# Optimization experiments

Measured on AMD Instinct MI355X. Metric: run time of the kernel, lower is better.

## Reference

```python
import jax, jax.numpy as jnp
import numpy as np

N, D, H = 3072, 1152, 16
HD = D // H  # 72


def setup_inputs() -> dict:
    key = jax.random.key(0)
    ks = jax.random.split(key, 12)
    w = lambda k, shp: jax.random.normal(k, shp, dtype=jnp.float32) * 0.02
    return {
        "hidden_states": jax.random.normal(ks[0], (N, D), dtype=jnp.float32),
        "rotary_pos_emb": jax.random.normal(ks[1], (N, HD // 2), dtype=jnp.float32),
        "cu_seqlens": jnp.arange(5, dtype=jnp.int32) * (N // 4),
        "wq": w(ks[2], (D, D)), "bq": jnp.zeros((D,), jnp.float32),
        "wk": w(ks[3], (D, D)), "bk": jnp.zeros((D,), jnp.float32),
        "wv": w(ks[4], (D, D)), "bv": jnp.zeros((D,), jnp.float32),
        "wo": w(ks[5], (D, D)), "bo": jnp.zeros((D,), jnp.float32),
    }


def _rotate_half(x):
    x1, x2 = jnp.split(x, 2, axis=-1)
    return jnp.concatenate((-x2, x1), axis=-1)


def _apply_rope(t, freqs):
    # t: [N, H, HD], freqs: [N, HD//2]
    cos = jnp.concatenate([jnp.cos(freqs), jnp.cos(freqs)], axis=-1)[:, None, :]  # [N,1,HD]
    sin = jnp.concatenate([jnp.sin(freqs), jnp.sin(freqs)], axis=-1)[:, None, :]
    return (t.astype(jnp.float32) * cos + _rotate_half(t.astype(jnp.float32)) * sin).astype(t.dtype)


def reference(hidden_states, rotary_pos_emb, cu_seqlens, wq, bq, wk, bk, wv, bv, wo, bo):
    n = hidden_states.shape[0]
    q = (hidden_states @ wq.T + bq).reshape(n, H, HD)
    k = (hidden_states @ wk.T + bk).reshape(n, H, HD)
    v = (hidden_states @ wv.T + bv).reshape(n, H, HD)
    q = _apply_rope(q, rotary_pos_emb)
    k = _apply_rope(k, rotary_pos_emb)
    # block-diagonal mask: same segment id (from cu_seqlens) -> attend
    seg = jnp.searchsorted(cu_seqlens, jnp.arange(n), side="right")
    same = seg[:, None] == seg[None, :]  # [N, N]
    neg = jnp.finfo(q.dtype).min
    scores = jnp.einsum("qhd,khd->hqk", q, k) / jnp.sqrt(jnp.float32(HD)).astype(q.dtype)
    scores = scores + jnp.where(same, jnp.zeros((), q.dtype), neg)[None, :, :]
    attn = jax.nn.softmax(scores.astype(jnp.float32), axis=-1).astype(q.dtype)
    out = jnp.einsum("hqk,khd->qhd", attn, v).reshape(n, D)
    return out @ wo.T + bo
```

## Files before the change

kernel.cpp:

```cpp
#include <hip/hip_runtime.h>
#include <hip/hip_bf16.h>


typedef __attribute__((ext_vector_type(8))) __bf16 bf16x8;
typedef __attribute__((ext_vector_type(4))) float f32x4;
typedef __attribute__((ext_vector_type(8))) unsigned short u16x8;
typedef __attribute__((ext_vector_type(4))) unsigned short u16x4;

#define N_TOK 3072
#define DMODEL 1152
#define NH 16
#define HDIM 72
#define SEGLEN 768

__device__ __forceinline__ unsigned short bf16rn(float f) {
  union { float f; unsigned int u; } v; v.f = f;
  return (unsigned short)((v.u + 0x7fffu + ((v.u >> 16) & 1u)) >> 16);
}
__device__ __forceinline__ float bf2f(unsigned short u) {
  union { unsigned int i; float f; } v; v.i = ((unsigned int)u) << 16;
  return v.f;
}

#define GLOAD16(gsrc, ldst)                                                  \
  __builtin_amdgcn_global_load_lds(                                         \
      (const __attribute__((address_space(1))) unsigned int*)(gsrc),        \
      (__attribute__((address_space(3))) unsigned int*)(ldst), 16, 0, 0)

__global__ __launch_bounds__(256) void prep_kernel(
    const float* __restrict__ hs,
    const float* __restrict__ wq, const float* __restrict__ wk,
    const float* __restrict__ wv, const float* __restrict__ wo,
    const float* __restrict__ bq, const float* __restrict__ bk,
    const float* __restrict__ bv,
    unsigned short* __restrict__ Xbf, unsigned short* __restrict__ Wqkv,
    unsigned short* __restrict__ Wo, float* __restrict__ biasqkv) {
  const int idx = blockIdx.x * 256 + threadIdx.x;
  const int stride = gridDim.x * 256;
  const int NX4 = (N_TOK * DMODEL) / 4;
  const int NW4 = (DMODEL * DMODEL) / 4;
  for (int i = idx; i < NX4; i += stride) {
    f32x4 v = ((const f32x4*)hs)[i];
    u16x4 o;
    for (int j = 0; j < 4; ++j) o[j] = bf16rn(v[j]);
    ((u16x4*)Xbf)[i] = o;
  }
  for (int i = idx; i < NW4; i += stride) {
    f32x4 a = ((const f32x4*)wq)[i];
    f32x4 b = ((const f32x4*)wk)[i];
    f32x4 c = ((const f32x4*)wv)[i];
    f32x4 d = ((const f32x4*)wo)[i];
    u16x4 oa, ob, oc, od;
    for (int j = 0; j < 4; ++j) {
      oa[j] = bf16rn(a[j]); ob[j] = bf16rn(b[j]);
      oc[j] = bf16rn(c[j]); od[j] = bf16rn(d[j]);
    }
    ((u16x4*)Wqkv)[i] = oa;
    ((u16x4*)(Wqkv + DMODEL * DMODEL))[i] = ob;
    ((u16x4*)(Wqkv + 2 * DMODEL * DMODEL))[i] = oc;
    ((u16x4*)Wo)[i] = od;
  }
  for (int i = idx; i < DMODEL; i += stride) {
    biasqkv[i] = bq[i];
    biasqkv[DMODEL + i] = bk[i];
    biasqkv[2 * DMODEL + i] = bv[i];
  }
}

template <int BM, int BN, int FM, int FN, bool OBF>
__global__ __launch_bounds__(256) void gemm_lds_kernel(
    const unsigned short* __restrict__ A, const unsigned short* __restrict__ B,
    const float* __restrict__ bias, void* __restrict__ Cout,
    int Nout, int K, int nbx) {
  __shared__ unsigned short As[2][BM * 32];
  __shared__ unsigned short Bs[2][BN * 32];
  const int t = threadIdx.x;
  const int lane = t & 63, wave = t >> 6;
  const int wr = wave >> 1, wc = wave & 1;
  const int g = lane >> 4, li = lane & 15;

  const int per = gridDim.x >> 3;
  const int gb = (blockIdx.x & 7) * per + (blockIdx.x >> 3);
  const int by = gb / nbx, bx = gb - by * nbx;
  const int bm = by * BM, bn = bx * BN;

  constexpr int LA = BM / 64;
  constexpr int LB = BN / 64;

  auto stage = [&](int buf, int kt) {
#pragma unroll
    for (int i = 0; i < LA; ++i) {
      const int s = i * 256 + t;
      const int row = s >> 2, cs = s & 3;
      const int gg = cs ^ ((row >> 1) & 3);
      GLOAD16(A + (long)(bm + row) * K + kt + gg * 8,
              &As[buf][(i * 256 + (t & ~63)) * 8]);
    }
#pragma unroll
    for (int i = 0; i < LB; ++i) {
      const int s = i * 256 + t;
      const int row = s >> 2, cs = s & 3;
      const int gg = cs ^ ((row >> 1) & 3);
      GLOAD16(B + (long)(bn + row) * K + kt + gg * 8,
              &Bs[buf][(i * 256 + (t & ~63)) * 8]);
    }
  };

  f32x4 acc[FM][FN];
#pragma unroll
  for (int i = 0; i < FM; ++i)
#pragma unroll
    for (int j = 0; j < FN; ++j) acc[i][j] = (f32x4)0.f;

  stage(0, 0);
  int cur = 0;
  const int nk = K / 32;
  for (int kt = 0; kt < nk; ++kt) {
    __syncthreads();
    if (kt + 1 < nk) stage(cur ^ 1, (kt + 1) * 32);
    bf16x8 af[FM], bf[FN];
#pragma unroll
    for (int i = 0; i < FM; ++i) {
      const int r = wr * (BM / 2) + i * 16 + li;
      af[i] = *(const bf16x8*)&As[cur][r * 32 + ((g ^ ((r >> 1) & 3)) * 8)];
    }
#pragma unroll
    for (int j = 0; j < FN; ++j) {
      const int r = wc * (BN / 2) + j * 16 + li;
      bf[j] = *(const bf16x8*)&Bs[cur][r * 32 + ((g ^ ((r >> 1) & 3)) * 8)];
    }
#pragma unroll
    for (int i = 0; i < FM; ++i)
#pragma unroll
      for (int j = 0; j < FN; ++j)
        acc[i][j] = __builtin_amdgcn_mfma_f32_16x16x32_bf16(af[i], bf[j],
                                                            acc[i][j], 0, 0, 0);
    cur ^= 1;
  }

#pragma unroll
  for (int i = 0; i < FM; ++i) {
    const int row = bm + wr * (BM / 2) + i * 16 + g * 4;
#pragma unroll
    for (int j = 0; j < FN; ++j) {
      const int col = bn + wc * (BN / 2) + j * 16 + li;
      const float bb = bias[col];
#pragma unroll
      for (int r = 0; r < 4; ++r) {
        const float v = acc[i][j][r] + bb;
        if constexpr (OBF)
          ((unsigned short*)Cout)[(long)(row + r) * Nout + col] = bf16rn(v);
        else
          ((float*)Cout)[(long)(row + r) * Nout + col] = v;
      }
    }
  }
}

__global__ __launch_bounds__(256) void rope_pack_kernel(
    const unsigned short* __restrict__ qkv, const float* __restrict__ rope,
    unsigned short* __restrict__ Qp, unsigned short* __restrict__ Kp,
    unsigned short* __restrict__ Vt) {
  const int nb = blockIdx.x;
  const int h = blockIdx.y;
  const int n0 = nb * 64;
  const int t = threadIdx.x;
  const float qscale = 0.11785113f;
  __shared__ float cs[64][36], sn[64][36];
  __shared__ float vtile[72][65];

  for (int i = t; i < 64 * 36; i += 256) {
    const int n = i / 36, d = i % 36;
    const float f = rope[(long)(n0 + n) * 36 + d];
    cs[n][d] = __cosf(f);
    sn[n][d] = __sinf(f);
  }
  __syncthreads();

  for (int i = t; i < 64 * 9; i += 256) {
    const int n = i / 9, dq = (i % 9) * 4;
    const long base = (long)(n0 + n) * 3456 + h * HDIM;
    u16x4 q1 = *(const u16x4*)&qkv[base + dq];
    u16x4 q2 = *(const u16x4*)&qkv[base + dq + 36];
    u16x4 k1 = *(const u16x4*)&qkv[base + DMODEL + dq];
    u16x4 k2 = *(const u16x4*)&qkv[base + DMODEL + dq + 36];
    u16x4 oq1, oq2, ok1, ok2;
#pragma unroll
    for (int e = 0; e < 4; ++e) {
      const float c = cs[n][dq + e], s = sn[n][dq + e];
      float f1 = bf2f(q1[e]), f2 = bf2f(q2[e]);
      oq1[e] = bf16rn((f1 * c - f2 * s) * qscale);
      oq2[e] = bf16rn((f2 * c + f1 * s) * qscale);
      f1 = bf2f(k1[e]); f2 = bf2f(k2[e]);
      ok1[e] = bf16rn(f1 * c - f2 * s);
      ok2[e] = bf16rn(f2 * c + f1 * s);
    }
    const long ob = ((long)h * N_TOK + n0 + n) * 96;
    *(u16x4*)&Qp[ob + dq] = oq1;
    *(u16x4*)&Qp[ob + dq + 36] = oq2;
    *(u16x4*)&Kp[ob + dq] = ok1;
    *(u16x4*)&Kp[ob + dq + 36] = ok2;
  }
  for (int i = t; i < 64 * 6; i += 256) {
    const int n = i / 6, dp = HDIM + (i % 6) * 4;
    const long ob = ((long)h * N_TOK + n0 + n) * 96;
    *(u16x4*)&Qp[ob + dp] = (u16x4)0;
    *(u16x4*)&Kp[ob + dp] = (u16x4)0;
  }
  for (int i = t; i < 64 * 9; i += 256) {
    const int n = i / 9, dq = (i % 9) * 8;
    u16x8 v = *(const u16x8*)&qkv[(long)(n0 + n) * 3456 + 2 * DMODEL + h * HDIM + dq];
#pragma unroll
    for (int e = 0; e < 8; ++e) vtile[dq + e][n] = bf2f(v[e]);
  }
  __syncthreads();
  for (int i = t; i < 80 * 8; i += 256) {
    const int d = i / 8, nq = (i % 8) * 8;
    u16x8 o;
#pragma unroll
    for (int e = 0; e < 8; ++e)
      o[e] = (d < HDIM) ? bf16rn(vtile[d][nq + e]) : (unsigned short)0;
    *(u16x8*)&Vt[((long)h * 80 + d) * N_TOK + n0 + nq] = o;
  }
}

__global__ __launch_bounds__(256) void attn_kernel(
    const unsigned short* __restrict__ Qp, const unsigned short* __restrict__ Kp,
    const unsigned short* __restrict__ Vt, unsigned short* __restrict__ AO) {
  const int b = blockIdx.x;
  const int hs = b & 63, qt = b >> 6;
  const int h = hs >> 2, seg = hs & 3;
  const int t = threadIdx.x;
  const int lane = t & 63, w = t >> 6;
  const int g = lane >> 4, li = lane & 15;

  __shared__ unsigned short Ks[2][64 * 96];
  __shared__ unsigned short Vs[2][80 * 64];
  __shared__ unsigned short Ps[4][16][72];

  const int q0 = seg * SEGLEN + qt * 64;
  const unsigned short* kbase = Kp + ((long)h * N_TOK + seg * SEGLEN) * 96;
  const unsigned short* vbase = Vt + (long)h * 80 * N_TOK + seg * SEGLEN;

  auto stageK = [&](int buf, int koff) {
#pragma unroll
    for (int i = 0; i < 3; ++i) {
      const int s = i * 256 + t;
      const int row = s / 12, c = s - row * 12;
      const int gg = c ^ ((row >> 1) & 3);
      GLOAD16(kbase + (long)(koff + row) * 96 + gg * 8,
              &Ks[buf][(i * 256 + (t & ~63)) * 8]);
    }
  };
  auto stageV = [&](int buf, int koff) {
#pragma unroll
    for (int i = 0; i < 2; ++i) {
      const int s = i * 256 + t;
      const int row = s >> 3, ch = s & 7;
      const int gg = ch ^ (row & 7);
      GLOAD16(vbase + (long)row * N_TOK + koff + gg * 8,
              &Vs[buf][(i * 256 + (t & ~63)) * 8]);
    }
    if (t < 128) {
      const int s = 512 + t;
      const int row = s >> 3, ch = s & 7;
      const int gg = ch ^ (row & 7);
      GLOAD16(vbase + (long)row * N_TOK + koff + gg * 8,
              &Vs[buf][(512 + (t & ~63)) * 8]);
    }
  };

  bf16x8 aq[3];
  {
    const unsigned short* qsrc = Qp + ((long)h * N_TOK + q0 + w * 16 + li) * 96;
#pragma unroll
    for (int c = 0; c < 3; ++c)
      aq[c] = *(const bf16x8*)(qsrc + c * 32 + g * 8);
  }

  f32x4 accO[5];
#pragma unroll
  for (int j = 0; j < 5; ++j) accO[j] = (f32x4)0.f;
  float l[4] = {0.f, 0.f, 0.f, 0.f};

  stageK(0, 0);
  stageV(0, 0);
  int cur = 0;
  for (int kv = 0; kv < 12; ++kv) {
    __syncthreads();
    if (kv + 1 < 12) {
      stageK(cur ^ 1, (kv + 1) * 64);
      stageV(cur ^ 1, (kv + 1) * 64);
    }

    f32x4 sc[4];
#pragma unroll
    for (int f = 0; f < 4; ++f) sc[f] = (f32x4)0.f;
#pragma unroll
    for (int c = 0; c < 3; ++c)
#pragma unroll
      for (int f = 0; f < 4; ++f) {
        const int kr = f * 16 + li;
        bf16x8 bk = *(const bf16x8*)
            &Ks[cur][kr * 96 + (((c * 4 + g) ^ ((kr >> 1) & 3)) * 8)];
        sc[f] = __builtin_amdgcn_mfma_f32_16x16x32_bf16(aq[c], bk, sc[f], 0, 0, 0);
      }

#pragma unroll
    for (int r = 0; r < 4; ++r) {
      float rs = 0.f;
#pragma unroll
      for (int f = 0; f < 4; ++f) {
        const float p = __expf(sc[f][r]);
        sc[f][r] = p;
        rs += p;
      }
      rs += __shfl_xor(rs, 1);
      rs += __shfl_xor(rs, 2);
      rs += __shfl_xor(rs, 4);
      rs += __shfl_xor(rs, 8);
      l[r] += rs;
#pragma unroll
      for (int f = 0; f < 4; ++f)
        Ps[w][g * 4 + r][f * 16 + li] = bf16rn(sc[f][r]);
    }

#pragma unroll
    for (int c = 0; c < 2; ++c) {
      bf16x8 ap = *(const bf16x8*)&Ps[w][li][c * 32 + g * 8];
#pragma unroll
      for (int j = 0; j < 5; ++j) {
        const int vr = j * 16 + li;
        bf16x8 bv = *(const bf16x8*)
            &Vs[cur][vr * 64 + (((c * 4 + g) ^ (vr & 7)) * 8)];
        accO[j] = __builtin_amdgcn_mfma_f32_16x16x32_bf16(ap, bv, accO[j], 0, 0, 0);
      }
    }
    cur ^= 1;
  }

#pragma unroll
  for (int j = 0; j < 5; ++j) {
    const int d = j * 16 + li;
    if (d < HDIM) {
#pragma unroll
      for (int r = 0; r < 4; ++r) {
        const int n = q0 + w * 16 + g * 4 + r;
        AO[(long)n * DMODEL + h * HDIM + d] = bf16rn(accO[j][r] / l[r]);
      }
    }
  }
}

extern "C" void kernel_launch(void* const* d_in, const int* in_sizes, int n_in,
                              void* d_out, int out_size, void* d_ws,
                              size_t ws_size, hipStream_t stream) {
  const float* hs = (const float*)d_in[0];
  const float* rope = (const float*)d_in[1];
  const float* wq = (const float*)d_in[3];
  const float* bq = (const float*)d_in[4];
  const float* wk = (const float*)d_in[5];
  const float* bk = (const float*)d_in[6];
  const float* wv = (const float*)d_in[7];
  const float* bv = (const float*)d_in[8];
  const float* wo = (const float*)d_in[9];
  const float* bo = (const float*)d_in[10];
  float* out = (float*)d_out;
  char* ws = (char*)d_ws;

  unsigned short* Xbf = (unsigned short*)(ws + 0);
  unsigned short* Wqkv = (unsigned short*)(ws + 7077888);
  unsigned short* Wo = (unsigned short*)(ws + 15040512);
  float* biasqkv = (float*)(ws + 17694720);
  unsigned short* qkvb = (unsigned short*)(ws + 17708544);
  unsigned short* Qp = (unsigned short*)(ws + 38942208);
  unsigned short* Kp = (unsigned short*)(ws + 48379392);
  unsigned short* Vt = (unsigned short*)(ws + 57816576);
  unsigned short* AO = (unsigned short*)(ws + 65680896);

  prep_kernel<<<dim3(1024), dim3(256), 0, stream>>>(
      hs, wq, wk, wv, wo, bq, bk, bv, Xbf, Wqkv, Wo, biasqkv);
  gemm_lds_kernel<128, 128, 4, 4, true><<<dim3(648), dim3(256), 0, stream>>>(
      Xbf, Wqkv, biasqkv, qkvb, 3 * DMODEL, DMODEL, 27);
  rope_pack_kernel<<<dim3(48, 16), dim3(256), 0, stream>>>(
      qkvb, rope, Qp, Kp, Vt);
  attn_kernel<<<dim3(768), dim3(256), 0, stream>>>(Qp, Kp, Vt, AO);
  gemm_lds_kernel<64, 128, 2, 4, false><<<dim3(432), dim3(256), 0, stream>>>(
      AO, Wo, bo, out, DMODEL, DMODEL, 9);
}
```

Before: 117.6 us.

## Split attention KV range in two blocks and combine partial outputs

Each attention block now handles half of the 768-key segment, using 32-key tiles and smaller LDS buffers, which doubles the grid to 1536 blocks. Unnormalized partial outputs and row sums go to workspace reused from the qkv buffer. A new combine kernel adds the two halves and divides by the summed normalizer. The aim is more parallelism and occupancy in attention, at the cost of an extra launch, partial-output traffic, and bf16 rounding of the partials.

```diff
diff --git a/kernel.cpp b/kernel.cpp
--- a/kernel.cpp
+++ b/kernel.cpp
@@ -226,47 +226,53 @@
 
 __global__ __launch_bounds__(256) void attn_kernel(
     const unsigned short* __restrict__ Qp, const unsigned short* __restrict__ Kp,
-    const unsigned short* __restrict__ Vt, unsigned short* __restrict__ AO) {
+    const unsigned short* __restrict__ Vt, unsigned short* __restrict__ pO,
+    float* __restrict__ pl) {
   const int b = blockIdx.x;
-  const int hs = b & 63, qt = b >> 6;
+  const int hs = b & 63, u = b >> 6;
   const int h = hs >> 2, seg = hs & 3;
+  const int qt = u >> 1, half = u & 1;
   const int t = threadIdx.x;
   const int lane = t & 63, w = t >> 6;
   const int g = lane >> 4, li = lane & 15;
 
-  __shared__ unsigned short Ks[2][64 * 96];
-  __shared__ unsigned short Vs[2][80 * 64];
-  __shared__ unsigned short Ps[4][16][72];
+  __shared__ unsigned short Ks[2][32 * 96];
+  __shared__ unsigned short Vs[2][80 * 32];
+  __shared__ unsigned short Ps[4][16][40];
 
   const int q0 = seg * SEGLEN + qt * 64;
+  const int koff0 = half * 384;
   const unsigned short* kbase = Kp + ((long)h * N_TOK + seg * SEGLEN) * 96;
   const unsigned short* vbase = Vt + (long)h * 80 * N_TOK + seg * SEGLEN;
 
   auto stageK = [&](int buf, int koff) {
-#pragma unroll
-    for (int i = 0; i < 3; ++i) {
-      const int s = i * 256 + t;
+    {
+      const int row = t / 12, c = t - row * 12;
+      const int gg = c ^ ((row >> 1) & 3);
+      GLOAD16(kbase + (long)(koff + row) * 96 + gg * 8,
+              &Ks[buf][(t & ~63) * 8]);
+    }
+    if (t < 128) {
+      const int s = 256 + t;
       const int row = s / 12, c = s - row * 12;
       const int gg = c ^ ((row >> 1) & 3);
       GLOAD16(kbase + (long)(koff + row) * 96 + gg * 8,
-              &Ks[buf][(i * 256 + (t & ~63)) * 8]);
+              &Ks[buf][(256 + (t & ~63)) * 8]);
     }
   };
   auto stageV = [&](int buf, int koff) {
-#pragma unroll
-    for (int i = 0; i < 2; ++i) {
-      const int s = i * 256 + t;
-      const int row = s >> 3, ch = s & 7;
-      const int gg = ch ^ (row & 7);
+    {
+      const int row = t >> 2, ch = t & 3;
+      const int gg = ch ^ ((row >> 1) & 3);
       GLOAD16(vbase + (long)row * N_TOK + koff + gg * 8,
-              &Vs[buf][(i * 256 + (t & ~63)) * 8]);
-    }
-    if (t < 128) {
-      const int s = 512 + t;
-      const int row = s >> 3, ch = s & 7;
-      const int gg = ch ^ (row & 7);
+              &Vs[buf][(t & ~63) * 8]);
+    }
+    if (t < 64) {
+      const int s = 256 + t;
+      const int row = s >> 2, ch = s & 3;
+      const int gg = ch ^ ((row >> 1) & 3);
       GLOAD16(vbase + (long)row * N_TOK + koff + gg * 8,
-              &Vs[buf][(512 + (t & ~63)) * 8]);
+              &Vs[buf][(256 + (t & ~63)) * 8]);
     }
   };
 
@@ -283,23 +289,23 @@
   for (int j = 0; j < 5; ++j) accO[j] = (f32x4)0.f;
   float l[4] = {0.f, 0.f, 0.f, 0.f};
 
-  stageK(0, 0);
-  stageV(0, 0);
+  stageK(0, koff0);
+  stageV(0, koff0);
   int cur = 0;
   for (int kv = 0; kv < 12; ++kv) {
     __syncthreads();
     if (kv + 1 < 12) {
-      stageK(cur ^ 1, (kv + 1) * 64);
-      stageV(cur ^ 1, (kv + 1) * 64);
-    }
-
-    f32x4 sc[4];
-#pragma unroll
-    for (int f = 0; f < 4; ++f) sc[f] = (f32x4)0.f;
+      stageK(cur ^ 1, koff0 + (kv + 1) * 32);
+      stageV(cur ^ 1, koff0 + (kv + 1) * 32);
+    }
+
+    f32x4 sc[2];
+#pragma unroll
+    for (int f = 0; f < 2; ++f) sc[f] = (f32x4)0.f;
 #pragma unroll
     for (int c = 0; c < 3; ++c)
 #pragma unroll
-      for (int f = 0; f < 4; ++f) {
+      for (int f = 0; f < 2; ++f) {
         const int kr = f * 16 + li;
         bf16x8 bk = *(const bf16x8*)
             &Ks[cur][kr * 96 + (((c * 4 + g) ^ ((kr >> 1) & 3)) * 8)];
@@ -308,48 +314,63 @@
 
 #pragma unroll
     for (int r = 0; r < 4; ++r) {
-      float rs = 0.f;
-#pragma unroll
-      for (int f = 0; f < 4; ++f) {
-        const float p = __expf(sc[f][r]);
-        sc[f][r] = p;
-        rs += p;
-      }
+      float p0 = __expf(sc[0][r]);
+      float p1 = __expf(sc[1][r]);
+      float rs = p0 + p1;
       rs += __shfl_xor(rs, 1);
       rs += __shfl_xor(rs, 2);
       rs += __shfl_xor(rs, 4);
       rs += __shfl_xor(rs, 8);
       l[r] += rs;
-#pragma unroll
-      for (int f = 0; f < 4; ++f)
-        Ps[w][g * 4 + r][f * 16 + li] = bf16rn(sc[f][r]);
-    }
-
-#pragma unroll
-    for (int c = 0; c < 2; ++c) {
-      bf16x8 ap = *(const bf16x8*)&Ps[w][li][c * 32 + g * 8];
+      Ps[w][g * 4 + r][li] = bf16rn(p0);
+      Ps[w][g * 4 + r][16 + li] = bf16rn(p1);
+    }
+
+    {
+      bf16x8 ap = *(const bf16x8*)&Ps[w][li][g * 8];
 #pragma unroll
       for (int j = 0; j < 5; ++j) {
         const int vr = j * 16 + li;
         bf16x8 bv = *(const bf16x8*)
-            &Vs[cur][vr * 64 + (((c * 4 + g) ^ (vr & 7)) * 8)];
+            &Vs[cur][vr * 32 + ((g ^ ((vr >> 1) & 3)) * 8)];
         accO[j] = __builtin_amdgcn_mfma_f32_16x16x32_bf16(ap, bv, accO[j], 0, 0, 0);
       }
     }
     cur ^= 1;
   }
 
+  const long pbase = ((long)(half * 16 + h)) * N_TOK;
 #pragma unroll
   for (int j = 0; j < 5; ++j) {
     const int d = j * 16 + li;
-    if (d < HDIM) {
-#pragma unroll
-      for (int r = 0; r < 4; ++r) {
-        const int n = q0 + w * 16 + g * 4 + r;
-        AO[(long)n * DMODEL + h * HDIM + d] = bf16rn(accO[j][r] / l[r]);
-      }
-    }
-  }
+#pragma unroll
+    for (int r = 0; r < 4; ++r) {
+      const int n = q0 + w * 16 + g * 4 + r;
+      pO[(pbase + n) * 80 + d] = bf16rn(accO[j][r]);
+    }
+  }
+  if (li == 0) {
+#pragma unroll
+    for (int r = 0; r < 4; ++r)
+      pl[pbase + q0 + w * 16 + g * 4 + r] = l[r];
+  }
+}
+
+__global__ __launch_bounds__(256) void combine_kernel(
+    const unsigned short* __restrict__ pO, const float* __restrict__ pl,
+    unsigned short* __restrict__ AO) {
+  const int idx = blockIdx.x * 256 + threadIdx.x;
+  const int row = idx / 9, q = idx - row * 9;
+  const long HS = (long)NH * N_TOK * 80;
+  u16x8 a = *(const u16x8*)&pO[(long)row * 80 + q * 8];
+  u16x8 b = *(const u16x8*)&pO[HS + (long)row * 80 + q * 8];
+  const float linv = 1.f / (pl[row] + pl[NH * N_TOK + row]);
+  const int h = row / N_TOK, n = row - h * N_TOK;
+  u16x8 o;
+#pragma unroll
+  for (int e = 0; e < 8; ++e)
+    o[e] = bf16rn((bf2f(a[e]) + bf2f(b[e])) * linv);
+  *(u16x8*)&AO[(long)n * DMODEL + h * HDIM + q * 8] = o;
 }
 
 extern "C" void kernel_launch(void* const* d_in, const int* in_sizes, int n_in,
@@ -373,6 +394,8 @@
   unsigned short* Wo = (unsigned short*)(ws + 15040512);
   float* biasqkv = (float*)(ws + 17694720);
   unsigned short* qkvb = (unsigned short*)(ws + 17708544);
+  unsigned short* pO = (unsigned short*)(ws + 17708544);
+  float* pl = (float*)(ws + 33437184);
   unsigned short* Qp = (unsigned short*)(ws + 38942208);
   unsigned short* Kp = (unsigned short*)(ws + 48379392);
   unsigned short* Vt = (unsigned short*)(ws + 57816576);
@@ -384,7 +407,8 @@
       Xbf, Wqkv, biasqkv, qkvb, 3 * DMODEL, DMODEL, 27);
   rope_pack_kernel<<<dim3(48, 16), dim3(256), 0, stream>>>(
       qkvb, rope, Qp, Kp, Vt);
-  attn_kernel<<<dim3(768), dim3(256), 0, stream>>>(Qp, Kp, Vt, AO);
+  attn_kernel<<<dim3(1536), dim3(256), 0, stream>>>(Qp, Kp, Vt, pO, pl);
+  combine_kernel<<<dim3(1728), dim3(256), 0, stream>>>(pO, pl, AO);
   gemm_lds_kernel<64, 128, 2, 4, false><<<dim3(432), dim3(256), 0, stream>>>(
       AO, Wo, bo, out, DMODEL, DMODEL, 9);
 }
```

New measurement: 125.8 us. +7.0%, slower.
